# Kernel tuning notes

Hardware: AMD Instinct MI355X
Metric: run time of the kernel (lower is better)

## Reference

```python
import jax, jax.numpy as jnp
import numpy as np

B, T, C, HD = 8, 2048, 1024, 64  # batch, seq, feature_size, head_dim = C // n_head


def setup_inputs() -> dict:
    key = jax.random.key(0)
    kx, kq, kk, kv = jax.random.split(key, 4)
    return {
        "x": jax.random.normal(kx, (B, T, C), dtype=jnp.float32),
        "Wq": jax.random.normal(kq, (C, HD), dtype=jnp.float32) * 0.02,
        "Wk": jax.random.normal(kk, (C, HD), dtype=jnp.float32) * 0.02,
        "Wv": jax.random.normal(kv, (C, HD), dtype=jnp.float32) * 0.02,
    }


def reference(x, Wq, Wk, Wv):
    # x: [B, T, C]; W*: [C, HD] (Linear(feature_size, feature_size//n_head, bias=False))
    Bsz, Tlen, Cdim = x.shape
    q = x @ Wq  # [B, T, HD]
    k = x @ Wk
    v = x @ Wv
    scores = jnp.einsum("btd,bsd->bts", q, k)  # [B, T, T]
    causal = jnp.tril(jnp.ones((Tlen, Tlen), dtype=bool))
    # faithful to source: masked_fill(-inf) THEN divide by sqrt(C) (full feature size)
    scores = jnp.where(causal, scores, -jnp.inf) / jnp.sqrt(jnp.float32(Cdim))
    att = jax.nn.softmax(scores, axis=-1)  # dropout p=0.0 (eval) -> identity
    return att @ v  # [B, T, HD]
```

## Files before the change

kernel.cpp:

```cpp
#include <hip/hip_runtime.h>


#define BATCH 8
#define SEQ   2048
#define CIN   1024
#define HDIM  64
#define NROW  (BATCH * SEQ)
#define UPB   136
#define NPB   (BATCH * UPB)

typedef __attribute__((ext_vector_type(8))) short bf16x8;
typedef __attribute__((ext_vector_type(4))) short u16x4;
typedef __attribute__((ext_vector_type(4))) float f32x4;

__device__ __forceinline__ unsigned short f2bf(float f) {
  unsigned int u = __builtin_bit_cast(unsigned int, f);
  u += 0x7fffu + ((u >> 16) & 1u);
  return (unsigned short)(u >> 16);
}
__device__ __forceinline__ float bf2f(unsigned short h) {
  return __builtin_bit_cast(float, (unsigned int)h << 16);
}
__device__ __forceinline__ u16x4 pack4(f32x4 a) {
  u16x4 r;
  r[0] = (short)f2bf(a[0]); r[1] = (short)f2bf(a[1]);
  r[2] = (short)f2bf(a[2]); r[3] = (short)f2bf(a[3]);
  return r;
}

__global__ __launch_bounds__(256) void wtrans_k(const float* __restrict__ wq,
                                                const float* __restrict__ wk,
                                                const float* __restrict__ wv,
                                                unsigned short* __restrict__ wt) {
  __shared__ unsigned short lds[64][65];
  const int m  = blockIdx.x >> 4;
  const int c0 = (blockIdx.x & 15) * 64;
  const float* w = (m == 0) ? wq : (m == 1) ? wk : wv;
  const int nl = threadIdx.x & 63, gr = threadIdx.x >> 6;
#pragma unroll
  for (int i = 0; i < 16; ++i) {
    int cl = gr * 16 + i;
    lds[cl][nl] = f2bf(w[(size_t)(c0 + cl) * HDIM + nl]);
  }
  __syncthreads();
#pragma unroll
  for (int i = 0; i < 16; ++i) {
    int n = gr * 16 + i;
    wt[(size_t)m * 65536 + n * CIN + c0 + nl] = lds[nl][n];
  }
}

__global__ __launch_bounds__(512) void qkv_proj_k(const float* __restrict__ x,
                                                  const unsigned short* __restrict__ wt,
                                                  unsigned short* __restrict__ q,
                                                  unsigned short* __restrict__ k,
                                                  unsigned short* __restrict__ vt) {
  __shared__ __align__(16) unsigned char ldsb[28672];
  const int tid  = threadIdx.x;
  const int lane = tid & 63;
  const int w    = tid >> 6;
  const int lr   = lane & 15, lg = lane >> 4;
  const int wm   = w & 1, wn = w >> 1;
  const int row0 = blockIdx.x * 32;

  const int trow  = tid >> 4;
  const int tcol4 = (tid & 15) * 4;
  const float* xg = x + (size_t)(row0 + trow) * CIN + tcol4;
  const int xoff  = trow * 128 + (((tcol4 >> 3) ^ (trow & 7)) << 4) + ((tcol4 & 4) << 1);

  const int wrow_ = tid >> 3;
  const int wg8   = tid & 7;
  const unsigned short* wg[3];
  int woff[3];
#pragma unroll
  for (int c = 0; c < 3; ++c) {
    int wrow = c * 64 + wrow_;
    wg[c]   = wt + (size_t)wrow * CIN + wg8 * 8;
    woff[c] = 4096 + wrow * 128 + ((wg8 ^ (wrow & 7)) << 4);
  }

  f32x4 acc[3];
#pragma unroll
  for (int i = 0; i < 3; ++i) acc[i] = (f32x4){0.f, 0.f, 0.f, 0.f};

  const int arow_off = (wm * 16 + lr) * 128;
  const int brow0    = wn * 48 + lr;

#pragma unroll 1
  for (int t = 0; t < 16; ++t) {
    const int k0 = t * 64;
    f32x4 xv = *(const f32x4*)(xg + k0);
    bf16x8 w0 = *(const bf16x8*)(wg[0] + k0);
    bf16x8 w1 = *(const bf16x8*)(wg[1] + k0);
    bf16x8 w2 = *(const bf16x8*)(wg[2] + k0);
    __syncthreads();
    *(u16x4*)(void*)(ldsb + xoff)    = pack4(xv);
    *(bf16x8*)(void*)(ldsb + woff[0]) = w0;
    *(bf16x8*)(void*)(ldsb + woff[1]) = w1;
    *(bf16x8*)(void*)(ldsb + woff[2]) = w2;
    __syncthreads();
#pragma unroll
    for (int kk = 0; kk < 2; ++kk) {
      const int swz = (((kk << 2) | lg) ^ (lr & 7)) << 4;
      bf16x8 af = *(const bf16x8*)(void*)(ldsb + arow_off + swz);
#pragma unroll
      for (int f = 0; f < 3; ++f) {
        bf16x8 bf_ = *(const bf16x8*)(void*)(ldsb + 4096 + (brow0 + f * 16) * 128 + swz);
        acc[f] = __builtin_amdgcn_mfma_f32_16x16x32_bf16(af, bf_, acc[f], 0, 0, 0);
      }
    }
  }

#pragma unroll
  for (int f = 0; f < 3; ++f) {
    const int gc  = wn * 48 + f * 16;
    const int mat = gc >> 6;
    const int hd  = (gc & 63) + lr;
#pragma unroll
    for (int j = 0; j < 4; ++j) {
      int grow = row0 + wm * 16 + lg * 4 + j;
      float v = acc[f][j];
      if (mat == 0) {
        q[(size_t)grow * HDIM + hd] = f2bf(v * 0.03125f);
      } else if (mat == 1) {
        k[(size_t)grow * HDIM + hd] = f2bf(v);
      } else {
        int b = grow >> 11, tp = grow & 2047;
        vt[((size_t)b * HDIM + hd) * SEQ + tp] = f2bf(v);
      }
    }
  }
}

__global__ __launch_bounds__(512) void attn_k(const unsigned short* __restrict__ q,
                                              const unsigned short* __restrict__ k,
                                              const unsigned short* __restrict__ vt,
                                              float* __restrict__ opart,
                                              float* __restrict__ m_l) {
  __shared__ __align__(16) unsigned char kv_lds[4][8192];
  __shared__ __align__(16) unsigned short plds[8][16][72];
  const int tid  = threadIdx.x;
  const int lane = tid & 63;
  const int w    = tid >> 6;
  const int lr = lane & 15, lg = lane >> 4, lr7 = lane & 7;

  const int blk = blockIdx.x;
  const int b   = blk / UPB;
  const int u   = blk - b * UPB;
  int i = 0;
#pragma unroll
  for (int j = 1; j <= 15; ++j) if (((j * (j + 1)) >> 1) <= u) i = j;
  const int seg  = u - ((i * (i + 1)) >> 1);
  const int r0   = i * 128 + w * 16;
  const int kvb  = seg * 128;
  const int p    = blk;

  const unsigned short* qb_ = q  + (size_t)b * SEQ * HDIM;
  const unsigned short* kb_ = k  + (size_t)b * SEQ * HDIM;
  const unsigned short* vb_ = vt + (size_t)b * HDIM * SEQ;

  const int srow = tid >> 3;
  const int sg   = tid & 7;
  const unsigned short* ks0 = kb_ + (size_t)(kvb + srow) * HDIM + sg * 8;
  const unsigned short* vs0 = vb_ + (size_t)srow * SEQ + kvb + sg * 8;
  bf16x8 kv0 = *(const bf16x8*)(ks0);
  bf16x8 vv0 = *(const bf16x8*)(vs0);
  bf16x8 kv1 = *(const bf16x8*)(ks0 + 64 * HDIM);
  bf16x8 vv1 = *(const bf16x8*)(vs0 + 64);
  bf16x8 qf0 = *(const bf16x8*)(qb_ + (size_t)(r0 + lr) * HDIM + lg * 8);
  bf16x8 qf1 = *(const bf16x8*)(qb_ + (size_t)(r0 + lr) * HDIM + 32 + lg * 8);
  const int soff = srow * 128 + ((sg ^ (srow & 7)) << 4);
  *(bf16x8*)(kv_lds[0] + soff) = kv0;
  *(bf16x8*)(kv_lds[1] + soff) = vv0;
  *(bf16x8*)(kv_lds[2] + soff) = kv1;
  *(bf16x8*)(kv_lds[3] + soff) = vv1;
  __syncthreads();

  f32x4 o[4];
#pragma unroll
  for (int n = 0; n < 4; ++n) o[n] = (f32x4){0.f, 0.f, 0.f, 0.f};
  float m_run = -INFINITY, l_run = 0.f;
  const int   qrow = r0 + lr;
  const float LOG2E = 1.44269504f;
  unsigned short (*pw)[72] = plds[w];

#pragma unroll 1
  for (int tt = 0; tt < 2; ++tt) {
    const int kv = kvb + tt * 64;
    if (kv > r0 + 15) continue;
    const unsigned char* Kt = kv_lds[tt * 2];
    const unsigned char* Vt = kv_lds[tt * 2 + 1];

    f32x4 sv[4];
#pragma unroll
    for (int f = 0; f < 4; ++f) {
      const int base = (f * 16 + lr) * 128;
      bf16x8 ka0 = *(const bf16x8*)(Kt + base + ((lg ^ lr7) << 4));
      bf16x8 ka1 = *(const bf16x8*)(Kt + base + (((4 + lg) ^ lr7) << 4));
      sv[f] = (f32x4){0.f, 0.f, 0.f, 0.f};
      sv[f] = __builtin_amdgcn_mfma_f32_16x16x32_bf16(ka0, qf0, sv[f], 0, 0, 0);
      sv[f] = __builtin_amdgcn_mfma_f32_16x16x32_bf16(ka1, qf1, sv[f], 0, 0, 0);
    }
    if (kv + 63 > r0) {
#pragma unroll
      for (int f = 0; f < 4; ++f)
#pragma unroll
        for (int j = 0; j < 4; ++j)
          if (kv + f * 16 + lg * 4 + j > qrow) sv[f][j] = -INFINITY;
    }
    float tm = -INFINITY;
#pragma unroll
    for (int f = 0; f < 4; ++f)
#pragma unroll
      for (int j = 0; j < 4; ++j) tm = fmaxf(tm, sv[f][j]);
    tm = fmaxf(tm, __shfl_xor(tm, 16, 64));
    tm = fmaxf(tm, __shfl_xor(tm, 32, 64));
    float m_new = fmaxf(m_run, tm);
    float alpha = (m_run == -INFINITY) ? 0.f : exp2f((m_run - m_new) * LOG2E);
    float mc    = (m_new == -INFINITY) ? 0.f : m_new * LOG2E;
    float ps = 0.f;
#pragma unroll
    for (int f = 0; f < 4; ++f) {
      float p0 = exp2f(sv[f][0] * LOG2E - mc);
      float p1 = exp2f(sv[f][1] * LOG2E - mc);
      float p2 = exp2f(sv[f][2] * LOG2E - mc);
      float p3 = exp2f(sv[f][3] * LOG2E - mc);
      ps += (p0 + p1) + (p2 + p3);
      unsigned int lo32 = (unsigned int)f2bf(p0) | ((unsigned int)f2bf(p1) << 16);
      unsigned int hi32 = (unsigned int)f2bf(p2) | ((unsigned int)f2bf(p3) << 16);
      uint2 pk; pk.x = lo32; pk.y = hi32;
      *(uint2*)(&pw[lr][f * 16 + lg * 4]) = pk;
    }
    ps += __shfl_xor(ps, 16, 64);
    ps += __shfl_xor(ps, 32, 64);
    l_run = l_run * alpha + ps;
    m_run = m_new;
#pragma unroll
    for (int j = 0; j < 4; ++j) {
      float aj = __shfl(alpha, lg * 4 + j, 64);
      o[0][j] *= aj; o[1][j] *= aj; o[2][j] *= aj; o[3][j] *= aj;
    }
    asm volatile("s_waitcnt lgkmcnt(0)" ::: "memory");
    __builtin_amdgcn_sched_barrier(0);
#pragma unroll
    for (int kk = 0; kk < 2; ++kk) {
      bf16x8 pf = *(const bf16x8*)(&pw[lr][kk * 32 + lg * 8]);
#pragma unroll
      for (int n = 0; n < 4; ++n) {
        bf16x8 vf = *(const bf16x8*)(Vt + (n * 16 + lr) * 128 + (((kk * 4 + lg) ^ lr7) << 4));
        o[n] = __builtin_amdgcn_mfma_f32_16x16x32_bf16(pf, vf, o[n], 0, 0, 0);
      }
    }
  }

  if (lane < 16) {
    m_l[p * 256 + w * 16 + lane]       = m_run;
    m_l[p * 256 + 128 + w * 16 + lane] = l_run;
  }
#pragma unroll
  for (int j = 0; j < 4; ++j) {
    int rloc = w * 16 + lg * 4 + j;
#pragma unroll
    for (int n = 0; n < 4; ++n)
      opart[(size_t)p * 8192 + rloc * 64 + n * 16 + lr] = o[n][j];
  }
}

__global__ __launch_bounds__(256) void combine_k(const float* __restrict__ opart,
                                                 const float* __restrict__ m_l,
                                                 float* __restrict__ out) {
  const float LOG2E = 1.44269504f;
  int idx = blockIdx.x * 256 + threadIdx.x;
  int col = idx & 63;
  int row = idx >> 6;
  int b = row >> 11, t = row & 2047;
  int i = t >> 7, r = t & 127;
  int S = i + 1;
  int pb = b * UPB + ((i * (i + 1)) >> 1);
  float M = -INFINITY;
  for (int s = 0; s < S; ++s) M = fmaxf(M, m_l[(pb + s) * 256 + r]);
  float l = 0.f, o = 0.f;
  for (int s = 0; s < S; ++s) {
    float ms = m_l[(pb + s) * 256 + r];
    float w  = exp2f((ms - M) * LOG2E);
    l += m_l[(pb + s) * 256 + 128 + r] * w;
    o += opart[(size_t)(pb + s) * 8192 + r * 64 + col] * w;
  }
  out[(size_t)row * HDIM + col] = o / l;
}

extern "C" void kernel_launch(void* const* d_in, const int* in_sizes, int n_in,
                              void* d_out, int out_size, void* d_ws, size_t ws_size,
                              hipStream_t stream) {
  const float* x  = (const float*)d_in[0];
  const float* wq = (const float*)d_in[1];
  const float* wk = (const float*)d_in[2];
  const float* wv = (const float*)d_in[3];
  float* outp = (float*)d_out;

  float* m_l   = (float*)d_ws;
  float* opart = m_l + (size_t)NPB * 256;
  unsigned short* qbuf = (unsigned short*)(opart + (size_t)NPB * 8192);
  unsigned short* kbuf = qbuf + (size_t)NROW * HDIM;
  unsigned short* vbuf = kbuf + (size_t)NROW * HDIM;
  unsigned short* wt   = vbuf + (size_t)NROW * HDIM;

  hipLaunchKernelGGL(wtrans_k, dim3(48), dim3(256), 0, stream, wq, wk, wv, wt);
  hipLaunchKernelGGL(qkv_proj_k, dim3(NROW / 32), dim3(512), 0, stream, x, wt, qbuf, kbuf, vbuf);
  hipLaunchKernelGGL(attn_k, dim3(NPB), dim3(512), 0, stream, qbuf, kbuf, vbuf, opart, m_l);
  hipLaunchKernelGGL(combine_k, dim3(NROW * HDIM / 256), dim3(256), 0, stream, opart, m_l, outp);
}
```

Measured before the change: 151.4 us.

## Double-buffer QKV projection LDS and double rows per block

The QKV projection kernel now processes 64 rows per block instead of 32, with each wave computing six MFMA tiles, so the weight tiles loaded into LDS are reused across twice as many rows. The LDS staging is double-buffered and the next K-step's global loads are issued after a single barrier, which removes one barrier per iteration and overlaps loads with MFMA work. The cost is more LDS (64 KB) and more registers per thread, which may lower occupancy. The grid is also halved, to 256 blocks.

```diff
diff --git a/kernel.cpp b/kernel.cpp
--- a/kernel.cpp
+++ b/kernel.cpp
@@ -21,10 +21,12 @@
 __device__ __forceinline__ float bf2f(unsigned short h) {
   return __builtin_bit_cast(float, (unsigned int)h << 16);
 }
-__device__ __forceinline__ u16x4 pack4(f32x4 a) {
-  u16x4 r;
+__device__ __forceinline__ bf16x8 pack8(f32x4 a, f32x4 b) {
+  bf16x8 r;
   r[0] = (short)f2bf(a[0]); r[1] = (short)f2bf(a[1]);
   r[2] = (short)f2bf(a[2]); r[3] = (short)f2bf(a[3]);
+  r[4] = (short)f2bf(b[0]); r[5] = (short)f2bf(b[1]);
+  r[6] = (short)f2bf(b[2]); r[7] = (short)f2bf(b[3]);
   return r;
 }
 
@@ -50,70 +52,69 @@
   }
 }
 
+#define QXB  8192
+#define QWB  24576
+#define QBUF 32768
 __global__ __launch_bounds__(512) void qkv_proj_k(const float* __restrict__ x,
                                                   const unsigned short* __restrict__ wt,
                                                   unsigned short* __restrict__ q,
                                                   unsigned short* __restrict__ k,
                                                   unsigned short* __restrict__ vt) {
-  __shared__ __align__(16) unsigned char ldsb[28672];
+  __shared__ __align__(16) unsigned char ldsb[2 * QBUF];
   const int tid  = threadIdx.x;
   const int lane = tid & 63;
   const int w    = tid >> 6;
-  const int lr   = lane & 15, lg = lane >> 4;
-  const int wm   = w & 1, wn = w >> 1;
-  const int row0 = blockIdx.x * 32;
-
-  const int trow  = tid >> 4;
-  const int tcol4 = (tid & 15) * 4;
-  const float* xg = x + (size_t)(row0 + trow) * CIN + tcol4;
-  const int xoff  = trow * 128 + (((tcol4 >> 3) ^ (trow & 7)) << 4) + ((tcol4 & 4) << 1);
-
-  const int wrow_ = tid >> 3;
-  const int wg8   = tid & 7;
-  const unsigned short* wg[3];
-  int woff[3];
-#pragma unroll
-  for (int c = 0; c < 3; ++c) {
-    int wrow = c * 64 + wrow_;
-    wg[c]   = wt + (size_t)wrow * CIN + wg8 * 8;
-    woff[c] = 4096 + wrow * 128 + ((wg8 ^ (wrow & 7)) << 4);
-  }
-
-  f32x4 acc[3];
-#pragma unroll
-  for (int i = 0; i < 3; ++i) acc[i] = (f32x4){0.f, 0.f, 0.f, 0.f};
-
-  const int arow_off = (wm * 16 + lr) * 128;
-  const int brow0    = wn * 48 + lr;
-
-#pragma unroll 1
+  const int lr   = lane & 15, lg = lane >> 4, lr7 = lane & 7;
+  const int wm   = w & 3, wn = w >> 2;
+  const int row0 = blockIdx.x * 64;
+
+  const int srow = tid >> 3;
+  const int sg   = tid & 7;
+  const float*          xg  = x  + (size_t)(row0 + srow) * CIN + sg * 8;
+  const unsigned short* wgp = wt + (size_t)srow * CIN + sg * 8;
+  const int soff = srow * 128 + ((sg ^ (srow & 7)) << 4);
+
+  f32x4 acc[6];
+#pragma unroll
+  for (int i = 0; i < 6; ++i) acc[i] = (f32x4){0.f, 0.f, 0.f, 0.f};
+
+  f32x4  xa = *(const f32x4*)(xg);
+  f32x4  xb = *(const f32x4*)(xg + 4);
+  bf16x8 w0 = *(const bf16x8*)(wgp);
+  bf16x8 w1 = *(const bf16x8*)(wgp + 64 * CIN);
+  bf16x8 w2 = *(const bf16x8*)(wgp + 128 * CIN);
+
+#pragma unroll 2
   for (int t = 0; t < 16; ++t) {
-    const int k0 = t * 64;
-    f32x4 xv = *(const f32x4*)(xg + k0);
-    bf16x8 w0 = *(const bf16x8*)(wg[0] + k0);
-    bf16x8 w1 = *(const bf16x8*)(wg[1] + k0);
-    bf16x8 w2 = *(const bf16x8*)(wg[2] + k0);
+    unsigned char* buf = ldsb + (t & 1) * QBUF;
+    *(bf16x8*)(buf + soff)               = pack8(xa, xb);
+    *(bf16x8*)(buf + QXB + soff)         = w0;
+    *(bf16x8*)(buf + QXB + soff + 8192)  = w1;
+    *(bf16x8*)(buf + QXB + soff + 16384) = w2;
     __syncthreads();
-    *(u16x4*)(void*)(ldsb + xoff)    = pack4(xv);
-    *(bf16x8*)(void*)(ldsb + woff[0]) = w0;
-    *(bf16x8*)(void*)(ldsb + woff[1]) = w1;
-    *(bf16x8*)(void*)(ldsb + woff[2]) = w2;
-    __syncthreads();
+    if (t < 15) {
+      const int k0 = (t + 1) * 64;
+      xa = *(const f32x4*)(xg + k0);
+      xb = *(const f32x4*)(xg + k0 + 4);
+      w0 = *(const bf16x8*)(wgp + k0);
+      w1 = *(const bf16x8*)(wgp + 64 * CIN + k0);
+      w2 = *(const bf16x8*)(wgp + 128 * CIN + k0);
+    }
 #pragma unroll
     for (int kk = 0; kk < 2; ++kk) {
-      const int swz = (((kk << 2) | lg) ^ (lr & 7)) << 4;
-      bf16x8 af = *(const bf16x8*)(void*)(ldsb + arow_off + swz);
-#pragma unroll
-      for (int f = 0; f < 3; ++f) {
-        bf16x8 bf_ = *(const bf16x8*)(void*)(ldsb + 4096 + (brow0 + f * 16) * 128 + swz);
+      const int swz = (((kk << 2) | lg) ^ lr7) << 4;
+      bf16x8 af = *(const bf16x8*)(void*)(buf + (wm * 16 + lr) * 128 + swz);
+#pragma unroll
+      for (int f = 0; f < 6; ++f) {
+        bf16x8 bf_ = *(const bf16x8*)(void*)(buf + QXB + (wn * 96 + f * 16 + lr) * 128 + swz);
         acc[f] = __builtin_amdgcn_mfma_f32_16x16x32_bf16(af, bf_, acc[f], 0, 0, 0);
       }
     }
   }
 
 #pragma unroll
-  for (int f = 0; f < 3; ++f) {
-    const int gc  = wn * 48 + f * 16;
+  for (int f = 0; f < 6; ++f) {
+    const int gc  = wn * 96 + f * 16;
     const int mat = gc >> 6;
     const int hd  = (gc & 63) + lr;
 #pragma unroll
@@ -306,7 +307,7 @@
   unsigned short* wt   = vbuf + (size_t)NROW * HDIM;
 
   hipLaunchKernelGGL(wtrans_k, dim3(48), dim3(256), 0, stream, wq, wk, wv, wt);
-  hipLaunchKernelGGL(qkv_proj_k, dim3(NROW / 32), dim3(512), 0, stream, x, wt, qbuf, kbuf, vbuf);
+  hipLaunchKernelGGL(qkv_proj_k, dim3(NROW / 64), dim3(512), 0, stream, x, wt, qbuf, kbuf, vbuf);
   hipLaunchKernelGGL(attn_k, dim3(NPB), dim3(512), 0, stream, qbuf, kbuf, vbuf, opart, m_l);
   hipLaunchKernelGGL(combine_k, dim3(NROW * HDIM / 256), dim3(256), 0, stream, opart, m_l, outp);
 }
```

Result: faster. 145.2 us (-4.1%).
